# Kernel optimization log

Hardware: AMD Instinct MI355X
Metric: run time of the kernel (lower is better)

Reference implementation:

```python
import jax, jax.numpy as jnp
import numpy as np

N = 100000      # nodes
E = 1600000     # edges (avg degree 16)
F_IN = 14       # Mutagenicity num_node_features
H = 64          # hidden_channels
C = 2           # Mutagenicity num_classes
G = 512         # graphs in batch


def setup_inputs() -> dict:
    key = jax.random.key(0)
    ks = jax.random.split(key, 16)
    x = jax.random.normal(ks[0], (N, F_IN), jnp.float32)
    edge_index = jax.random.randint(ks[1], (2, E), 0, N, dtype=jnp.int32)
    batch = jnp.sort(jax.random.randint(ks[2], (N,), 0, G, dtype=jnp.int32))
    def lin(k, fi, fo):
        bound = 1.0 / np.sqrt(fi)
        kw, kb = jax.random.split(k)
        W = jax.random.uniform(kw, (fi, fo), jnp.float32, -bound, bound)
        b = jax.random.uniform(kb, (fo,), jnp.float32, -bound, bound)
        return W, b
    W1, b1 = lin(ks[3], F_IN, H)
    W2, b2 = lin(ks[4], H, H)
    W3, b3 = lin(ks[5], H, H)
    W4, b4 = lin(ks[6], H, H)
    W5, b5 = lin(ks[7], H, H)
    Wlin, blin = lin(ks[8], H, C)
    return {"x": x, "W1": W1, "b1": b1, "W2": W2, "b2": b2, "W3": W3, "b3": b3,
            "W4": W4, "b4": b4, "W5": W5, "b5": b5, "Wlin": Wlin, "blin": blin,
            "edge_index": edge_index, "batch": batch}


def _gcn_conv(h, W, b, src, dst, norm, dinv):
    # PyG GCNConv: out = D^{-1/2}(A+I)D^{-1/2} (h W) + b
    m = h @ W                                              # [N, Fout]
    agg = jax.ops.segment_sum(m[src] * norm[:, None], dst, num_segments=N)
    agg = agg + m * dinv[:, None]                          # self-loop term (norm = 1/deg)
    return agg + b


def reference(x, W1, b1, W2, b2, W3, b3, W4, b4, W5, b5, Wlin, blin, edge_index, batch):
    src, dst = edge_index[0], edge_index[1]
    # degree with self-loops (counted on target nodes, source_to_target flow)
    deg = jax.ops.segment_sum(jnp.ones(E, jnp.float32), dst, num_segments=N) + 1.0
    dinv_sqrt = jax.lax.rsqrt(deg)
    norm = dinv_sqrt[src] * dinv_sqrt[dst]                 # per-edge weight
    dinv = dinv_sqrt * dinv_sqrt                           # self-loop weight 1/deg

    h = jax.nn.relu(_gcn_conv(x, W1, b1, src, dst, norm, dinv))
    h = jax.nn.relu(_gcn_conv(h, W2, b2, src, dst, norm, dinv))
    h = jax.nn.relu(_gcn_conv(h, W3, b3, src, dst, norm, dinv))
    h = jax.nn.relu(_gcn_conv(h, W4, b4, src, dst, norm, dinv))
    h = jax.nn.relu(_gcn_conv(h, W5, b5, src, dst, norm, dinv))

    pooled = jax.ops.segment_max(h, batch, num_segments=G)  # [G, H]
    return pooled @ Wlin + blin                             # [G, C]
```

## Files before the change

### kernel.cpp

```cpp
#include <hip/hip_runtime.h>
#include <hip/hip_bf16.h>


#define HDIM 64
#define SCAN_CHUNK 1024
#define FILL_S 8


__global__ __launch_bounds__(256) void count_sharded(const int* __restrict__ dst,
                                                     int* __restrict__ deg,
                                                     int E, int shard_w, int nchunks) {
    int shard = blockIdx.x & (FILL_S - 1);
    int chunk = blockIdx.x >> 3;
    int epc = (E + nchunks - 1) / nchunks;
    int e0 = chunk * epc;
    int e1 = min(e0 + epc, E);
    int lo = shard * shard_w, hi = lo + shard_w;
    for (int e = e0 + (int)threadIdx.x; e < e1; e += 256) {
        int d = dst[e];
        if (d >= lo && d < hi) atomicAdd(&deg[d], 1);
    }
}

__global__ __launch_bounds__(256) void partial_sums(const int* __restrict__ deg,
                                                    int* __restrict__ psum, int n) {
    __shared__ int red[256];
    int base = blockIdx.x * SCAN_CHUNK;
    int s = 0;
    #pragma unroll
    for (int j = 0; j < 4; ++j) {
        int i = base + j * 256 + threadIdx.x;
        if (i < n) s += deg[i];
    }
    red[threadIdx.x] = s;
    __syncthreads();
    for (int off = 128; off > 0; off >>= 1) {
        if (threadIdx.x < off) red[threadIdx.x] += red[threadIdx.x + off];
        __syncthreads();
    }
    if (threadIdx.x == 0) psum[blockIdx.x] = red[0];
}

__global__ __launch_bounds__(128) void scan_partials(int* __restrict__ psum, int nb) {
    __shared__ int tmp[128];
    int t = threadIdx.x;
    int v = (t < nb) ? psum[t] : 0;
    tmp[t] = v;
    __syncthreads();
    for (int off = 1; off < 128; off <<= 1) {
        int u = (t >= off) ? tmp[t - off] : 0;
        __syncthreads();
        tmp[t] += u;
        __syncthreads();
    }
    if (t < nb) psum[t] = tmp[t] - v;
}

__global__ __launch_bounds__(256) void scan_final(const int* __restrict__ deg,
                                                  const int* __restrict__ psum,
                                                  int* __restrict__ rowptr, int n) {
    __shared__ int ts[256];
    int t = threadIdx.x;
    int base = blockIdx.x * SCAN_CHUNK + t * 4;
    int v[4];
    int s = 0;
    #pragma unroll
    for (int j = 0; j < 4; ++j) {
        int i = base + j;
        v[j] = (i < n) ? deg[i] : 0;
        s += v[j];
    }
    ts[t] = s;
    __syncthreads();
    int mine = s;
    for (int off = 1; off < 256; off <<= 1) {
        int u = (t >= off) ? ts[t - off] : 0;
        __syncthreads();
        ts[t] += u;
        __syncthreads();
    }
    int ex = ts[t] - mine + psum[blockIdx.x];
    #pragma unroll
    for (int j = 0; j < 4; ++j) {
        int i = base + j;
        if (i < n) rowptr[i] = ex;
        ex += v[j];
    }
}

__global__ __launch_bounds__(256) void node_arrays(const int* __restrict__ deg,
                                                   const int* __restrict__ rowptr,
                                                   float* __restrict__ ds,
                                                   int* __restrict__ cursor, int n) {
    int i = blockIdx.x * blockDim.x + threadIdx.x;
    if (i < n) {
        float d = (float)(deg[i] + 1);
        ds[i] = 1.0f / sqrtf(d);
        cursor[i] = rowptr[i];
    }
}

__global__ __launch_bounds__(256) void fill_csr_sharded(const int* __restrict__ src,
                                                        const int* __restrict__ dst,
                                                        int* __restrict__ cursor,
                                                        int* __restrict__ csr_src,
                                                        int E, int shard_w, int nchunks) {
    int shard = blockIdx.x & (FILL_S - 1);
    int chunk = blockIdx.x >> 3;
    int epc = (E + nchunks - 1) / nchunks;
    int e0 = chunk * epc;
    int e1 = min(e0 + epc, E);
    int lo = shard * shard_w, hi = lo + shard_w;
    for (int e = e0 + (int)threadIdx.x; e < e1; e += 256) {
        int d = dst[e];
        if (d >= lo && d < hi) {
            int pos = atomicAdd(&cursor[d], 1);
            csr_src[pos] = src[e];
        }
    }
}

__global__ __launch_bounds__(256) void pad_scale_x(const float* __restrict__ x,
                                                   const float* __restrict__ ds,
                                                   float* __restrict__ xp, int n_nodes) {
    int idx = blockIdx.x * blockDim.x + threadIdx.x;
    if (idx >= n_nodes * 16) return;
    int n = idx >> 4, j = idx & 15;
    xp[idx] = (j < 14) ? x[n * 14 + j] * ds[n] : 0.0f;
}


__global__ __launch_bounds__(256) void gather16(const float* __restrict__ xp,
                                               const int* __restrict__ rowptr,
                                               const int* __restrict__ cnt,
                                               const int* __restrict__ csr_src,
                                               const float* __restrict__ ds,
                                               float* __restrict__ agg16, int n_nodes) {
    int lane = threadIdx.x & 63;
    int sub = lane >> 4, l = lane & 15;
    int wave = blockIdx.x * (blockDim.x >> 6) + (threadIdx.x >> 6);
    int node = wave * 4 + sub;
    if (node >= n_nodes) return;
    float dsn = ds[node];
    float a0 = xp[node * 16 + l];
    float a1 = 0.f, a2 = 0.f, a3 = 0.f;
    int s = rowptr[node];
    int e = s + cnt[node];
    int i = s;
    for (; i + 3 < e; i += 4) {
        int s0 = csr_src[i], s1 = csr_src[i + 1], s2 = csr_src[i + 2], s3 = csr_src[i + 3];
        a0 += xp[s0 * 16 + l];
        a1 += xp[s1 * 16 + l];
        a2 += xp[s2 * 16 + l];
        a3 += xp[s3 * 16 + l];
    }
    for (; i < e; ++i) a0 += xp[csr_src[i] * 16 + l];
    agg16[node * 16 + l] = ((a0 + a1) + (a2 + a3)) * dsn;
}


template <int K, int KW, bool BIAS_RELU, bool SCALE>
__global__ __launch_bounds__(256) void matmul_k(const float* __restrict__ h,
                                                const float* __restrict__ W,
                                                const float* __restrict__ bias,
                                                const float* __restrict__ ds,
                                                float* __restrict__ m, int n_nodes) {
    __shared__ float ldsbuf[4 * 4 * K];
    int lane = threadIdx.x & 63;
    int wv = threadIdx.x >> 6;
    int wave = blockIdx.x * 4 + wv;
    int n0 = wave * 4;
    if (n0 >= n_nodes) return;
    float wcol[K];
    #pragma unroll
    for (int k = 0; k < K; ++k) wcol[k] = (k < KW) ? W[k * HDIM + lane] : 0.f;
    float bl = BIAS_RELU ? bias[lane] : 0.f;

    if (n0 + 3 < n_nodes) {
        float* myl = &ldsbuf[wv * 4 * K];
        const float4* src4 = reinterpret_cast<const float4*>(h + (size_t)n0 * K);
        if constexpr (K == 64) {
            reinterpret_cast<float4*>(myl)[lane] = src4[lane];
        } else {
            if (lane < K) reinterpret_cast<float4*>(myl)[lane] = src4[lane];
        }
        const float4* r0 = reinterpret_cast<const float4*>(myl + 0 * K);
        const float4* r1 = reinterpret_cast<const float4*>(myl + 1 * K);
        const float4* r2 = reinterpret_cast<const float4*>(myl + 2 * K);
        const float4* r3 = reinterpret_cast<const float4*>(myl + 3 * K);
        float a0[4] = {0, 0, 0, 0}, a1[4] = {0, 0, 0, 0};
        float a2[4] = {0, 0, 0, 0}, a3[4] = {0, 0, 0, 0};
        #pragma unroll
        for (int k4 = 0; k4 < K / 4; ++k4) {
            int c = k4 & 3;
            float4 v0 = r0[k4], v1 = r1[k4], v2 = r2[k4], v3 = r3[k4];
            float w0 = wcol[4 * k4 + 0], w1 = wcol[4 * k4 + 1];
            float w2 = wcol[4 * k4 + 2], w3 = wcol[4 * k4 + 3];
            a0[c] += v0.x * w0 + v0.y * w1 + v0.z * w2 + v0.w * w3;
            a1[c] += v1.x * w0 + v1.y * w1 + v1.z * w2 + v1.w * w3;
            a2[c] += v2.x * w0 + v2.y * w1 + v2.z * w2 + v2.w * w3;
            a3[c] += v3.x * w0 + v3.y * w1 + v3.z * w2 + v3.w * w3;
        }
        float s0 = (a0[0] + a0[1]) + (a0[2] + a0[3]);
        float s1 = (a1[0] + a1[1]) + (a1[2] + a1[3]);
        float s2 = (a2[0] + a2[1]) + (a2[2] + a2[3]);
        float s3 = (a3[0] + a3[1]) + (a3[2] + a3[3]);
        if constexpr (BIAS_RELU) {
            s0 = fmaxf(s0 + bl, 0.f);
            s1 = fmaxf(s1 + bl, 0.f);
            s2 = fmaxf(s2 + bl, 0.f);
            s3 = fmaxf(s3 + bl, 0.f);
        }
        if constexpr (SCALE) {
            s0 *= ds[n0 + 0];
            s1 *= ds[n0 + 1];
            s2 *= ds[n0 + 2];
            s3 *= ds[n0 + 3];
        }
        m[(size_t)(n0 + 0) * HDIM + lane] = s0;
        m[(size_t)(n0 + 1) * HDIM + lane] = s1;
        m[(size_t)(n0 + 2) * HDIM + lane] = s2;
        m[(size_t)(n0 + 3) * HDIM + lane] = s3;
    } else {
        for (int n = n0; n < n_nodes; ++n) {
            const float4* hrow = reinterpret_cast<const float4*>(h + (size_t)n * K);
            float acc[4] = {0, 0, 0, 0};
            #pragma unroll
            for (int k4 = 0; k4 < K / 4; ++k4) {
                float4 hv = hrow[k4];
                acc[k4 & 3] += hv.x * wcol[4 * k4 + 0] + hv.y * wcol[4 * k4 + 1] +
                               hv.z * wcol[4 * k4 + 2] + hv.w * wcol[4 * k4 + 3];
            }
            float s = (acc[0] + acc[1]) + (acc[2] + acc[3]);
            if constexpr (BIAS_RELU) s = fmaxf(s + bl, 0.f);
            if constexpr (SCALE) s *= ds[n];
            m[(size_t)n * HDIM + lane] = s;
        }
    }
}


__global__ __launch_bounds__(256) void gcn_gather(const float* __restrict__ m,
                                                  const int* __restrict__ rowptr,
                                                  const int* __restrict__ cnt,
                                                  const int* __restrict__ csr_src,
                                                  const float* __restrict__ ds,
                                                  const float* __restrict__ bias,
                                                  float* __restrict__ hout, int n_nodes) {
    int lane = threadIdx.x & 63;
    int node = blockIdx.x * (blockDim.x >> 6) + (threadIdx.x >> 6);
    if (node >= n_nodes) return;
    float dsn = ds[node];
    float a0 = m[node * HDIM + lane];
    float a1 = 0.f, a2 = 0.f, a3 = 0.f;
    float a4 = 0.f, a5 = 0.f, a6 = 0.f, a7 = 0.f;
    int s = rowptr[node];
    int e = s + cnt[node];
    int i = s;
    for (; i + 15 < e; i += 16) {
        int t0 = csr_src[i],      t1 = csr_src[i + 1],  t2 = csr_src[i + 2],  t3 = csr_src[i + 3];
        int t4 = csr_src[i + 4],  t5 = csr_src[i + 5],  t6 = csr_src[i + 6],  t7 = csr_src[i + 7];
        int t8 = csr_src[i + 8],  t9 = csr_src[i + 9],  ta = csr_src[i + 10], tb = csr_src[i + 11];
        int tc = csr_src[i + 12], td = csr_src[i + 13], te = csr_src[i + 14], tf = csr_src[i + 15];
        a0 += m[t0 * HDIM + lane];
        a1 += m[t1 * HDIM + lane];
        a2 += m[t2 * HDIM + lane];
        a3 += m[t3 * HDIM + lane];
        a4 += m[t4 * HDIM + lane];
        a5 += m[t5 * HDIM + lane];
        a6 += m[t6 * HDIM + lane];
        a7 += m[t7 * HDIM + lane];
        a0 += m[t8 * HDIM + lane];
        a1 += m[t9 * HDIM + lane];
        a2 += m[ta * HDIM + lane];
        a3 += m[tb * HDIM + lane];
        a4 += m[tc * HDIM + lane];
        a5 += m[td * HDIM + lane];
        a6 += m[te * HDIM + lane];
        a7 += m[tf * HDIM + lane];
    }
    for (; i + 7 < e; i += 8) {
        int t0 = csr_src[i],     t1 = csr_src[i + 1], t2 = csr_src[i + 2], t3 = csr_src[i + 3];
        int t4 = csr_src[i + 4], t5 = csr_src[i + 5], t6 = csr_src[i + 6], t7 = csr_src[i + 7];
        a0 += m[t0 * HDIM + lane];
        a1 += m[t1 * HDIM + lane];
        a2 += m[t2 * HDIM + lane];
        a3 += m[t3 * HDIM + lane];
        a4 += m[t4 * HDIM + lane];
        a5 += m[t5 * HDIM + lane];
        a6 += m[t6 * HDIM + lane];
        a7 += m[t7 * HDIM + lane];
    }
    for (; i + 1 < e; i += 2) {
        int t0 = csr_src[i], t1 = csr_src[i + 1];
        a0 += m[t0 * HDIM + lane];
        a1 += m[t1 * HDIM + lane];
    }
    if (i < e) a0 += m[csr_src[i] * HDIM + lane];
    float v = ((a0 + a1) + (a2 + a3) + ((a4 + a5) + (a6 + a7))) * dsn + bias[lane];
    hout[node * HDIM + lane] = fmaxf(v, 0.f);
}


__global__ __launch_bounds__(256) void pool_linear(const float* __restrict__ h,
                                                   const int* __restrict__ batch,
                                                   const float* __restrict__ Wlin,
                                                   const float* __restrict__ blin,
                                                   float* __restrict__ out,
                                                   int n_nodes, int n_graphs) {
    int lane = threadIdx.x & 63;
    int g = blockIdx.x * (blockDim.x >> 6) + (threadIdx.x >> 6);
    if (g >= n_graphs) return;
    int lo = 0, hi = n_nodes;
    while (lo < hi) { int mid = (lo + hi) >> 1; if (batch[mid] < g) lo = mid + 1; else hi = mid; }
    int start = lo;
    hi = n_nodes;
    while (lo < hi) { int mid = (lo + hi) >> 1; if (batch[mid] < g + 1) lo = mid + 1; else hi = mid; }
    int end = lo;
    float vmax = 0.f;
    for (int n = start; n < end; ++n) vmax = fmaxf(vmax, h[(size_t)n * HDIM + lane]);
    float p0 = vmax * Wlin[lane * 2 + 0];
    float p1 = vmax * Wlin[lane * 2 + 1];
    #pragma unroll
    for (int off = 32; off > 0; off >>= 1) {
        p0 += __shfl_xor(p0, off);
        p1 += __shfl_xor(p1, off);
    }
    if (lane == 0) {
        out[g * 2 + 0] = p0 + blin[0];
        out[g * 2 + 1] = p1 + blin[1];
    }
}


extern "C" void kernel_launch(void* const* d_in, const int* in_sizes, int n_in,
                              void* d_out, int out_size, void* d_ws, size_t ws_size,
                              hipStream_t stream) {
    const float* x    = (const float*)d_in[0];
    const float* W1   = (const float*)d_in[1];
    const float* b1   = (const float*)d_in[2];
    const float* W2   = (const float*)d_in[3];
    const float* b2   = (const float*)d_in[4];
    const float* W3   = (const float*)d_in[5];
    const float* b3   = (const float*)d_in[6];
    const float* W4   = (const float*)d_in[7];
    const float* b4   = (const float*)d_in[8];
    const float* W5   = (const float*)d_in[9];
    const float* b5   = (const float*)d_in[10];
    const float* Wlin = (const float*)d_in[11];
    const float* blin = (const float*)d_in[12];
    const int* edge_index = (const int*)d_in[13];
    const int* batch      = (const int*)d_in[14];

    const int N = in_sizes[0] / 14;
    const int E = in_sizes[13] / 2;
    const int G = out_size / 2;
    const int* srcp = edge_index;
    const int* dstp = edge_index + E;

    char* ws = (char*)d_ws;
    size_t off = 0;
    auto alloc = [&](size_t bytes) -> void* {
        void* p = ws + off;
        off = (off + bytes + 255) & ~(size_t)255;
        return p;
    };
    int*   deg     = (int*)alloc((size_t)N * 4);
    int*   rowptr  = (int*)alloc((size_t)N * 4);
    int*   cursor  = (int*)alloc((size_t)N * 4);
    int*   psum    = (int*)alloc(128 * 4);
    float* ds      = (float*)alloc((size_t)N * 4);
    int*   csr_src = (int*)alloc((size_t)E * 4);
    float* buf_m   = (float*)alloc((size_t)N * HDIM * 4);
    float* buf_h   = (float*)alloc((size_t)N * HDIM * 4);
    (void)ws_size;
    float* xp    = buf_h;
    float* agg16 = buf_m;

    const int NB = (N + SCAN_CHUNK - 1) / SCAN_CHUNK;
    const int fill_chunks = 512;
    const int shard_w = (N + FILL_S - 1) / FILL_S;

    hipMemsetAsync(deg, 0, (size_t)N * 4, stream);
    count_sharded<<<fill_chunks * FILL_S, 256, 0, stream>>>(dstp, deg, E, shard_w, fill_chunks);
    partial_sums<<<NB, 256, 0, stream>>>(deg, psum, N);
    scan_partials<<<1, 128, 0, stream>>>(psum, NB);
    scan_final<<<NB, 256, 0, stream>>>(deg, psum, rowptr, N);
    node_arrays<<<(N + 255) / 256, 256, 0, stream>>>(deg, rowptr, ds, cursor, N);
    pad_scale_x<<<(N * 16 + 255) / 256, 256, 0, stream>>>(x, ds, xp, N);
    fill_csr_sharded<<<fill_chunks * FILL_S, 256, 0, stream>>>(srcp, dstp, cursor, csr_src,
                                                               E, shard_w, fill_chunks);

    const int gemm_blocks = (N + 15) / 16;
    const int gather_blocks = (N + 3) / 4;
    const int g16_blocks = (N + 15) / 16;

    gather16<<<g16_blocks, 256, 0, stream>>>(xp, rowptr, deg, csr_src, ds, agg16, N);
    matmul_k<16, 14, true, false><<<gemm_blocks, 256, 0, stream>>>(agg16, W1, b1, ds, buf_h, N);

    matmul_k<64, 64, false, true><<<gemm_blocks, 256, 0, stream>>>(buf_h, W2, b2, ds, buf_m, N);
    gcn_gather<<<gather_blocks, 256, 0, stream>>>(buf_m, rowptr, deg, csr_src, ds, b2, buf_h, N);
    matmul_k<64, 64, false, true><<<gemm_blocks, 256, 0, stream>>>(buf_h, W3, b3, ds, buf_m, N);
    gcn_gather<<<gather_blocks, 256, 0, stream>>>(buf_m, rowptr, deg, csr_src, ds, b3, buf_h, N);
    matmul_k<64, 64, false, true><<<gemm_blocks, 256, 0, stream>>>(buf_h, W4, b4, ds, buf_m, N);
    gcn_gather<<<gather_blocks, 256, 0, stream>>>(buf_m, rowptr, deg, csr_src, ds, b4, buf_h, N);
    matmul_k<64, 64, false, true><<<gemm_blocks, 256, 0, stream>>>(buf_h, W5, b5, ds, buf_m, N);
    gcn_gather<<<gather_blocks, 256, 0, stream>>>(buf_m, rowptr, deg, csr_src, ds, b5, buf_h, N);

    pool_linear<<<(G + 3) / 4, 256, 0, stream>>>(buf_h, batch, Wlin, blin, (float*)d_out, N, G);
}
```

Measured before the change: 704.3 us.

## Pre-partition edges by destination shard before CSR degree count and fill

Replaces the sharded count and fill passes, in which every shard scans all E edges and filters by destination range, with a bucket pass. Edges are first partitioned into 8 destination-range buckets using block histograms and global cursors. Count and fill then read only their shard's contiguous slice. This cuts redundant reads of dst from 8x per pass, at the cost of extra partition kernels and writes of pdst/psrc into the reused buf_m scratch.

```diff
diff --git a/kernel.cpp b/kernel.cpp
--- a/kernel.cpp
+++ b/kernel.cpp
@@ -5,21 +5,98 @@
 #define HDIM 64
 #define SCAN_CHUNK 1024
 #define FILL_S 8
-
-
-__global__ __launch_bounds__(256) void count_sharded(const int* __restrict__ dst,
-                                                     int* __restrict__ deg,
-                                                     int E, int shard_w, int nchunks) {
+#define PART_CH 2048
+
+
+__device__ __forceinline__ int shard_of(int d, int shard_w) {
+    int b = d / shard_w;
+    return b > (FILL_S - 1) ? (FILL_S - 1) : b;
+}
+
+__global__ __launch_bounds__(256) void bucket_count(const int* __restrict__ dst,
+                                                    int* __restrict__ bsize,
+                                                    int E, int shard_w) {
+    __shared__ int hist[FILL_S];
+    int t = threadIdx.x, lane = t & 63;
+    if (t < FILL_S) hist[t] = 0;
+    __syncthreads();
+    int e0 = blockIdx.x * PART_CH;
+    int e1 = min(e0 + PART_CH, E);
+    int c[FILL_S] = {0, 0, 0, 0, 0, 0, 0, 0};
+    for (int e = e0 + t; e < e1; e += 256) c[shard_of(dst[e], shard_w)]++;
+    #pragma unroll
+    for (int b = 0; b < FILL_S; ++b) {
+        int v = c[b];
+        v += __shfl_xor(v, 1);  v += __shfl_xor(v, 2);  v += __shfl_xor(v, 4);
+        v += __shfl_xor(v, 8);  v += __shfl_xor(v, 16); v += __shfl_xor(v, 32);
+        if (lane == 0) atomicAdd(&hist[b], v);
+    }
+    __syncthreads();
+    if (t < FILL_S && hist[t] > 0) atomicAdd(&bsize[t], hist[t]);
+}
+
+__global__ __launch_bounds__(64) void bucket_scan(const int* __restrict__ bsize,
+                                                  int* __restrict__ bbase,
+                                                  int* __restrict__ gcur) {
+    if (threadIdx.x == 0) {
+        int run = 0;
+        #pragma unroll
+        for (int i = 0; i < FILL_S; ++i) {
+            bbase[i] = run;
+            gcur[i] = run;
+            run += bsize[i];
+        }
+        bbase[FILL_S] = run;
+    }
+}
+
+__global__ __launch_bounds__(256) void edge_partition(const int* __restrict__ dst,
+                                                      const int* __restrict__ src,
+                                                      int* __restrict__ gcur,
+                                                      int* __restrict__ pdst,
+                                                      int* __restrict__ psrc,
+                                                      int E, int shard_w) {
+    __shared__ int hist[FILL_S];
+    __shared__ int base[FILL_S];
+    __shared__ int cnt2[FILL_S];
+    int t = threadIdx.x, lane = t & 63;
+    if (t < FILL_S) { hist[t] = 0; cnt2[t] = 0; }
+    __syncthreads();
+    int e0 = blockIdx.x * PART_CH;
+    int e1 = min(e0 + PART_CH, E);
+    int c[FILL_S] = {0, 0, 0, 0, 0, 0, 0, 0};
+    for (int e = e0 + t; e < e1; e += 256) c[shard_of(dst[e], shard_w)]++;
+    #pragma unroll
+    for (int b = 0; b < FILL_S; ++b) {
+        int v = c[b];
+        v += __shfl_xor(v, 1);  v += __shfl_xor(v, 2);  v += __shfl_xor(v, 4);
+        v += __shfl_xor(v, 8);  v += __shfl_xor(v, 16); v += __shfl_xor(v, 32);
+        if (lane == 0) atomicAdd(&hist[b], v);
+    }
+    __syncthreads();
+    if (t < FILL_S) base[t] = (hist[t] > 0) ? atomicAdd(&gcur[t], hist[t]) : 0;
+    __syncthreads();
+    for (int e = e0 + t; e < e1; e += 256) {
+        int d = dst[e];
+        int b = shard_of(d, shard_w);
+        int p = base[b] + atomicAdd(&cnt2[b], 1);
+        pdst[p] = d;
+        psrc[p] = src[e];
+    }
+}
+
+__global__ __launch_bounds__(256) void count_part(const int* __restrict__ pdst,
+                                                  const int* __restrict__ bbase,
+                                                  int* __restrict__ deg, int nchunks) {
     int shard = blockIdx.x & (FILL_S - 1);
     int chunk = blockIdx.x >> 3;
-    int epc = (E + nchunks - 1) / nchunks;
-    int e0 = chunk * epc;
-    int e1 = min(e0 + epc, E);
-    int lo = shard * shard_w, hi = lo + shard_w;
-    for (int e = e0 + (int)threadIdx.x; e < e1; e += 256) {
-        int d = dst[e];
-        if (d >= lo && d < hi) atomicAdd(&deg[d], 1);
-    }
+    int lo = bbase[shard], hi = bbase[shard + 1];
+    int len = hi - lo;
+    int epc = (len + nchunks - 1) / nchunks;
+    int e0 = lo + chunk * epc;
+    int e1 = min(e0 + epc, hi);
+    for (int e = e0 + (int)threadIdx.x; e < e1; e += 256)
+        atomicAdd(&deg[pdst[e]], 1);
 }
 
 __global__ __launch_bounds__(256) void partial_sums(const int* __restrict__ deg,
@@ -100,23 +177,22 @@
     }
 }
 
-__global__ __launch_bounds__(256) void fill_csr_sharded(const int* __restrict__ src,
-                                                        const int* __restrict__ dst,
-                                                        int* __restrict__ cursor,
-                                                        int* __restrict__ csr_src,
-                                                        int E, int shard_w, int nchunks) {
+__global__ __launch_bounds__(256) void fill_part(const int* __restrict__ pdst,
+                                                 const int* __restrict__ psrc,
+                                                 const int* __restrict__ bbase,
+                                                 int* __restrict__ cursor,
+                                                 int* __restrict__ csr_src, int nchunks) {
     int shard = blockIdx.x & (FILL_S - 1);
     int chunk = blockIdx.x >> 3;
-    int epc = (E + nchunks - 1) / nchunks;
-    int e0 = chunk * epc;
-    int e1 = min(e0 + epc, E);
-    int lo = shard * shard_w, hi = lo + shard_w;
+    int lo = bbase[shard], hi = bbase[shard + 1];
+    int len = hi - lo;
+    int epc = (len + nchunks - 1) / nchunks;
+    int e0 = lo + chunk * epc;
+    int e1 = min(e0 + epc, hi);
     for (int e = e0 + (int)threadIdx.x; e < e1; e += 256) {
-        int d = dst[e];
-        if (d >= lo && d < hi) {
-            int pos = atomicAdd(&cursor[d], 1);
-            csr_src[pos] = src[e];
-        }
+        int d = pdst[e];
+        int pos = atomicAdd(&cursor[d], 1);
+        csr_src[pos] = psrc[e];
     }
 }
 
@@ -369,6 +445,9 @@
     int*   rowptr  = (int*)alloc((size_t)N * 4);
     int*   cursor  = (int*)alloc((size_t)N * 4);
     int*   psum    = (int*)alloc(128 * 4);
+    int*   bsize   = (int*)alloc(16 * 4);
+    int*   bbase   = (int*)alloc(16 * 4);
+    int*   gcur    = (int*)alloc(16 * 4);
     float* ds      = (float*)alloc((size_t)N * 4);
     int*   csr_src = (int*)alloc((size_t)E * 4);
     float* buf_m   = (float*)alloc((size_t)N * HDIM * 4);
@@ -376,20 +455,27 @@
     (void)ws_size;
     float* xp    = buf_h;
     float* agg16 = buf_m;
+    int*   pdst  = (int*)buf_m;
+    int*   psrc  = (int*)buf_m + E;
 
     const int NB = (N + SCAN_CHUNK - 1) / SCAN_CHUNK;
     const int fill_chunks = 512;
     const int shard_w = (N + FILL_S - 1) / FILL_S;
+    const int part_blocks = (E + PART_CH - 1) / PART_CH;
 
     hipMemsetAsync(deg, 0, (size_t)N * 4, stream);
-    count_sharded<<<fill_chunks * FILL_S, 256, 0, stream>>>(dstp, deg, E, shard_w, fill_chunks);
+    hipMemsetAsync(bsize, 0, 16 * 4, stream);
+    bucket_count<<<part_blocks, 256, 0, stream>>>(dstp, bsize, E, shard_w);
+    bucket_scan<<<1, 64, 0, stream>>>(bsize, bbase, gcur);
+    edge_partition<<<part_blocks, 256, 0, stream>>>(dstp, srcp, gcur, pdst, psrc, E, shard_w);
+    count_part<<<fill_chunks * FILL_S, 256, 0, stream>>>(pdst, bbase, deg, fill_chunks);
     partial_sums<<<NB, 256, 0, stream>>>(deg, psum, N);
     scan_partials<<<1, 128, 0, stream>>>(psum, NB);
     scan_final<<<NB, 256, 0, stream>>>(deg, psum, rowptr, N);
     node_arrays<<<(N + 255) / 256, 256, 0, stream>>>(deg, rowptr, ds, cursor, N);
     pad_scale_x<<<(N * 16 + 255) / 256, 256, 0, stream>>>(x, ds, xp, N);
-    fill_csr_sharded<<<fill_chunks * FILL_S, 256, 0, stream>>>(srcp, dstp, cursor, csr_src,
-                                                               E, shard_w, fill_chunks);
+    fill_part<<<fill_chunks * FILL_S, 256, 0, stream>>>(pdst, psrc, bbase, cursor,
+                                                        csr_src, fill_chunks);
 
     const int gemm_blocks = (N + 15) / 16;
     const int gather_blocks = (N + 3) / 4;
```

After: 738.9 us. +4.9%, slower.
